# Kernel tuning notes

Measured on AMD Instinct MI355X. Metric: run time of the kernel, lower is better.

## Reference

```python
import jax, jax.numpy as jnp
import numpy as np

B, S, H = 4, 2048, 1024
NH, HD = 16, 64  # num heads, head dim


def setup_inputs() -> dict:
    key = jax.random.key(0)
    ks = jax.random.split(key, 8)
    s = 1.0 / np.sqrt(H)
    return {
        "hidden_states": jax.random.normal(ks[0], (B, S, H), jnp.float32),
        "attention_mask": jnp.zeros((B, 1, 1, S), jnp.float32),
        "Wq": jax.random.normal(ks[1], (H, H), jnp.float32) * s,
        "bq": jnp.zeros((H,), jnp.float32),
        "Wk": jax.random.normal(ks[2], (H, H), jnp.float32) * s,
        "bk": jnp.zeros((H,), jnp.float32),
        "Wv": jax.random.normal(ks[3], (H, H), jnp.float32) * s,
        "bv": jnp.zeros((H,), jnp.float32),
    }


def _split_heads(x):
    # [B, S, H] -> [B, NH, S, HD]
    return x.reshape(B, S, NH, HD).transpose(0, 2, 1, 3)


def reference(hidden_states, attention_mask, Wq, bq, Wk, bk, Wv, bv):
    q = _split_heads(hidden_states @ Wq + bq)
    k = _split_heads(hidden_states @ Wk + bk)
    v = _split_heads(hidden_states @ Wv + bv)
    scores = jnp.einsum("bhqd,bhkd->bhqk", q, k) / jnp.sqrt(jnp.float32(HD))
    probs = jax.nn.softmax(scores + attention_mask, axis=-1)  # dropout p=0 -> identity
    ctx = jnp.einsum("bhqk,bhkd->bhqd", probs, v)
    ctx = ctx.transpose(0, 2, 1, 3).reshape(B, S, H)
    return (ctx,)
```

## Files before the change

### kernel.cpp

```cpp
#include <hip/hip_runtime.h>
#include <hip/hip_bf16.h>
#include <stdint.h>


typedef unsigned short ushort_t;
typedef __attribute__((ext_vector_type(4))) float f32x4;
typedef __attribute__((ext_vector_type(8))) short short8;
typedef __attribute__((ext_vector_type(2))) unsigned int uint2v;

#define MFMA16(a, b, c) __builtin_amdgcn_mfma_f32_16x16x32_bf16((a), (b), (c), 0, 0, 0)

__device__ __forceinline__ ushort_t f2bf(float f) {
  unsigned u = __float_as_uint(f);
  u = (u + 0x7FFFu + ((u >> 16) & 1u)) >> 16;
  return (ushort_t)u;
}

typedef __attribute__((address_space(1))) unsigned int as1_uint;
typedef __attribute__((address_space(3))) unsigned int as3_uint;

__device__ __forceinline__ void async16(void* lds_dst, const void* g_src) {
  __builtin_amdgcn_global_load_lds((as1_uint*)(uintptr_t)g_src,
                                   (as3_uint*)(unsigned)(uintptr_t)lds_dst, 16, 0, 0);
}

__global__ __launch_bounds__(256) void convert_x(const float* __restrict__ X,
                                                 ushort_t* __restrict__ Xb) {
  int idx = (blockIdx.x * 256 + threadIdx.x) * 8;
  f32x4 a = *(const f32x4*)(X + idx);
  f32x4 b = *(const f32x4*)(X + idx + 4);
  short8 r;
#pragma unroll
  for (int j = 0; j < 4; ++j) r[j] = (short)f2bf(a[j]);
#pragma unroll
  for (int j = 0; j < 4; ++j) r[4 + j] = (short)f2bf(b[j]);
  *(short8*)(Xb + idx) = r;
}

__global__ __launch_bounds__(256) void convert_w(const float* __restrict__ Wq,
                                                 const float* __restrict__ Wk,
                                                 const float* __restrict__ Wv,
                                                 ushort_t* __restrict__ Wt) {
  const int mat = blockIdx.z;
  const float* W = (mat == 0) ? Wq : ((mat == 1) ? Wk : Wv);
  const int k0 = blockIdx.x * 64, n0 = blockIdx.y * 64;
  __shared__ float t[64][65];
  const int tid = threadIdx.x;
#pragma unroll
  for (int it = 0; it < 16; ++it) {
    int idx = it * 256 + tid;
    int r = idx >> 6, c = idx & 63;
    t[r][c] = W[(size_t)(k0 + r) * 1024 + n0 + c];
  }
  __syncthreads();
#pragma unroll
  for (int it = 0; it < 16; ++it) {
    int idx = it * 256 + tid;
    int nr = idx >> 6, kc = idx & 63;
    Wt[(size_t)(mat * 1024 + n0 + nr) * 1024 + k0 + kc] = f2bf(t[kc][nr]);
  }
}

__global__ __launch_bounds__(256) void gemm_qkv(const ushort_t* __restrict__ Xb,
                                                const ushort_t* __restrict__ Wt,
                                                const float* __restrict__ bq,
                                                const float* __restrict__ bk,
                                                const float* __restrict__ bv,
                                                ushort_t* __restrict__ Qb,
                                                ushort_t* __restrict__ Kb,
                                                ushort_t* __restrict__ Vt) {
  __shared__ char lds[36864];
  const int tid = threadIdx.x;
  const int l = tid & 63, w = tid >> 6;
  const int m0 = blockIdx.x * 128;
  const int n0 = blockIdx.y * 128;
  const int wm = w >> 1, wn = w & 1;

  const int lr = l >> 3;
  const int kb_log = (((l & 7) ^ lr) << 4);
  const char* srcA = (const char*)Xb + (size_t)(m0 + w * 32 + lr) * 2048 + kb_log;
  const char* srcB = (const char*)Wt + (size_t)(n0 + w * 32 + lr) * 2048 + kb_log;
  char* ldsA_w = lds + w * 4096;
  char* ldsB_w = lds + 16384 + w * 4096;

  const int ra = wm * 64 + (l & 15);
  const int rb = wn * 64 + (l & 15);
  const int swz = (l & 7) << 4;
  const int x0 = (((l >> 4) << 4)) ^ swz;
  const int x1 = (64 + ((l >> 4) << 4)) ^ swz;

  f32x4 acc[4][4];
#pragma unroll
  for (int mf = 0; mf < 4; ++mf)
#pragma unroll
    for (int nf = 0; nf < 4; ++nf) acc[mf][nf] = (f32x4){0.f, 0.f, 0.f, 0.f};

#pragma unroll 1
  for (int kt = 0; kt < 16; ++kt) {
    if (kt) __syncthreads();
    const int koff = kt * 128;
#pragma unroll
    for (int c = 0; c < 4; ++c) {
      async16(ldsA_w + c * 1024, srcA + c * 16384 + koff);
      async16(ldsB_w + c * 1024, srcB + c * 16384 + koff);
    }
    __syncthreads();
#pragma unroll
    for (int half = 0; half < 2; ++half) {
      const int xo = half ? x1 : x0;
      short8 av[4], bv2[4];
#pragma unroll
      for (int mf = 0; mf < 4; ++mf)
        av[mf] = *(const short8*)(lds + (ra + mf * 16) * 128 + xo);
#pragma unroll
      for (int nf = 0; nf < 4; ++nf)
        bv2[nf] = *(const short8*)(lds + 16384 + (rb + nf * 16) * 128 + xo);
#pragma unroll
      for (int mf = 0; mf < 4; ++mf)
#pragma unroll
        for (int nf = 0; nf < 4; ++nf)
          acc[mf][nf] = MFMA16(av[mf], bv2[nf], acc[mf][nf]);
    }
  }

  __syncthreads();
  const int col0 = n0 + wn * 64;
  const int mat = col0 >> 10;
  const int nn0 = col0 & 1023;
  const int hh = nn0 >> 6;
  const int row0 = m0 + wm * 64;
  const int bb = row0 >> 11;
  const int s0 = row0 & 2047;
  const float* bias = (mat == 0) ? bq : ((mat == 1) ? bk : bv);
  const float qscale = 0.18033688011112042f;
  if (mat < 2) {
    ushort_t* dst = (mat == 0) ? Qb : Kb;
    const float scl = (mat == 0) ? qscale : 1.0f;
#pragma unroll
    for (int mf = 0; mf < 4; ++mf)
#pragma unroll
      for (int nf = 0; nf < 4; ++nf)
#pragma unroll
        for (int i = 0; i < 4; ++i) {
          int r = mf * 16 + (l >> 4) * 4 + i;
          int d = nf * 16 + (l & 15);
          float v = (acc[mf][nf][i] + bias[nn0 + d]) * scl;
          dst[((size_t)(bb * 16 + hh) * 2048 + (s0 + r)) * 64 + d] = f2bf(v);
        }
  } else {
    ushort_t* vw = (ushort_t*)(lds + w * 9216);
#pragma unroll
    for (int mf = 0; mf < 4; ++mf)
#pragma unroll
      for (int nf = 0; nf < 4; ++nf)
#pragma unroll
        for (int i = 0; i < 4; ++i) {
          int r = mf * 16 + (l >> 4) * 4 + i;
          int d = nf * 16 + (l & 15);
          float v = acc[mf][nf][i] + bias[nn0 + d];
          vw[d * 72 + r] = f2bf(v);
        }
#pragma unroll
    for (int it = 0; it < 8; ++it) {
      int dr = it * 8 + (l >> 3);
      int sc = (l & 7) * 8;
      short8 vv = *(const short8*)((const char*)vw + dr * 144 + sc * 2);
      *(short8*)((char*)Vt + (((size_t)(bb * 16 + hh) * 64 + dr) * 2048 + s0 + sc) * 2) = vv;
    }
  }
}

__global__ __launch_bounds__(256) void attn_fwd(const ushort_t* __restrict__ Qb,
                                                const ushort_t* __restrict__ Kb,
                                                const ushort_t* __restrict__ Vt,
                                                const float* __restrict__ mask,
                                                float* __restrict__ out) {
  __shared__ char lds[49408];
  const int tid = threadIdx.x, l = tid & 63, w = tid >> 6;
  const int bh = blockIdx.y;
  const int bb = bh >> 4, hh = bh & 15;
  const int q0 = blockIdx.x * 64;
  const int lg = l >> 4, lr = l & 15;
  char* klds = lds;
  char* vlds = lds + 16384;
  char* pl = lds + 32768 + w * 2048;
  float* ml = (float*)(lds + 40960);
  float* sbuf = (float*)(lds + 49152 + w * 64);

  const float LOG2E = 1.44269504088896340736f;
  const f32x4 fzero = (f32x4){0.f, 0.f, 0.f, 0.f};
  const int psz = (lr & 7) << 4;

  const char* qbase = (const char*)Qb + ((size_t)bh * 2048 + q0 + w * 16 + lr) * 128 + lg * 16;
  short8 aq0 = *(const short8*)(qbase);
  short8 aq1 = *(const short8*)(qbase + 64);

  const int srow = l >> 3;
  const int scol = ((l & 7) ^ srow) << 4;
  const char* ksrc0 = (const char*)Kb + (size_t)bh * 2048 * 128 + (size_t)(w * 16 + srow) * 128 + scol;
  const char* vsrc0 = (const char*)Vt + ((size_t)bh * 64 + w * 16 + srow) * 4096 + scol;

  {
    char* kd = klds + w * 2048;
    char* vd = vlds + w * 2048;
    async16(kd, ksrc0);
    async16(kd + 1024, ksrc0 + 1024);
    async16(vd, vsrc0);
    async16(vd + 1024, vsrc0 + 8 * 4096);
  }
  {
    const float* mrow = mask + (size_t)bb * 2048;
    int mi = tid * 8;
    f32x4 a = *(const f32x4*)(mrow + mi);
    f32x4 b = *(const f32x4*)(mrow + mi + 4);
#pragma unroll
    for (int j = 0; j < 4; ++j) { a[j] *= LOG2E; b[j] *= LOG2E; }
    *(f32x4*)(ml + mi) = a;
    *(f32x4*)(ml + mi + 4) = b;
  }

  f32x4 lsum = fzero;
  f32x4 o[4];
#pragma unroll
  for (int vf = 0; vf < 4; ++vf) o[vf] = fzero;

#pragma unroll 1
  for (int kt = 0; kt < 32; ++kt) {
    const int cur = kt & 1;
    asm volatile("s_waitcnt lgkmcnt(0)" ::: "memory");
    __builtin_amdgcn_s_barrier();
    if (kt < 31) {
      char* kd = klds + (cur ^ 1) * 8192 + w * 2048;
      char* vd = vlds + (cur ^ 1) * 8192 + w * 2048;
      const char* ks = ksrc0 + (size_t)(kt + 1) * 8192;
      const char* vs = vsrc0 + (kt + 1) * 128;
      async16(kd, ks);
      async16(kd + 1024, ks + 1024);
      async16(vd, vs);
      async16(vd + 1024, vs + 8 * 4096);
      asm volatile("s_waitcnt vmcnt(4)" ::: "memory");
    } else {
      asm volatile("s_waitcnt vmcnt(0)" ::: "memory");
    }
    __builtin_amdgcn_s_barrier();
    __builtin_amdgcn_sched_barrier(0);

    const char* kb = klds + cur * 8192;
    const char* vb = vlds + cur * 8192;

#pragma unroll
    for (int kf = 0; kf < 4; ++kf) {
      const char* ka = kb + (kf * 16 + lr) * 128;
      short8 a0 = *(const short8*)(ka + ((lg * 16) ^ psz));
      short8 a1 = *(const short8*)(ka + ((64 + lg * 16) ^ psz));
      f32x4 s = MFMA16(a0, aq0, fzero);
      s = MFMA16(a1, aq1, s);
      f32x4 m4 = *(const f32x4*)(ml + kt * 64 + kf * 16 + lg * 4);
      f32x4 ps;
#pragma unroll
      for (int i = 0; i < 4; ++i) ps[i] = __builtin_amdgcn_exp2f(s[i] + m4[i]);
      lsum += ps;
      unsigned w0, w1;
      asm("v_cvt_pk_bf16_f32 %0, %1, %2" : "=v"(w0) : "v"(ps[0]), "v"(ps[1]));
      asm("v_cvt_pk_bf16_f32 %0, %1, %2" : "=v"(w1) : "v"(ps[2]), "v"(ps[3]));
      uint2v pw2 = {w0, w1};
      *(uint2v*)(pl + lr * 128 + ((kf * 32 + lg * 8) ^ psz)) = pw2;
    }

    short8 pa0 = *(const short8*)(pl + lr * 128 + ((lg * 16) ^ psz));
    short8 pa1 = *(const short8*)(pl + lr * 128 + ((64 + lg * 16) ^ psz));
#pragma unroll
    for (int vf = 0; vf < 4; ++vf) {
      const char* vrow = vb + (vf * 16 + lr) * 128;
      short8 v0 = *(const short8*)(vrow + ((lg * 16) ^ psz));
      short8 v1 = *(const short8*)(vrow + ((64 + lg * 16) ^ psz));
      o[vf] = MFMA16(pa0, v0, o[vf]);
      o[vf] = MFMA16(pa1, v1, o[vf]);
    }
  }

  float lrun = (lsum[0] + lsum[1]) + (lsum[2] + lsum[3]);
  lrun += __shfl_xor(lrun, 16);
  lrun += __shfl_xor(lrun, 32);
  if (lg == 0) sbuf[lr] = lrun;
  f32x4 l4 = *(const f32x4*)(sbuf + lg * 4);
  f32x4 inv4;
#pragma unroll
  for (int i = 0; i < 4; ++i) inv4[i] = 1.0f / l4[i];
#pragma unroll
  for (int vf = 0; vf < 4; ++vf)
#pragma unroll
    for (int i = 0; i < 4; ++i)
      out[((size_t)bb * 2048 + q0 + w * 16 + lg * 4 + i) * 1024 + hh * 64 + vf * 16 + lr] =
          o[vf][i] * inv4[i];
}

extern "C" void kernel_launch(void* const* d_in, const int* in_sizes, int n_in,
                              void* d_out, int out_size, void* d_ws, size_t ws_size,
                              hipStream_t stream) {
  const float* hs  = (const float*)d_in[0];
  const float* msk = (const float*)d_in[1];
  const float* Wq  = (const float*)d_in[2];
  const float* bq  = (const float*)d_in[3];
  const float* Wk  = (const float*)d_in[4];
  const float* bk  = (const float*)d_in[5];
  const float* Wv  = (const float*)d_in[6];
  const float* bv  = (const float*)d_in[7];
  float* out = (float*)d_out;
  char* ws = (char*)d_ws;
  ushort_t* Xb = (ushort_t*)ws;
  ushort_t* Wt = (ushort_t*)(ws + (16u << 20));
  ushort_t* Qb = (ushort_t*)(ws + (22u << 20));
  ushort_t* Kb = (ushort_t*)(ws + (38u << 20));
  ushort_t* Vt = (ushort_t*)(ws + (54u << 20));

  convert_x<<<4096, 256, 0, stream>>>(hs, Xb);
  convert_w<<<dim3(16, 16, 3), 256, 0, stream>>>(Wq, Wk, Wv, Wt);
  gemm_qkv<<<dim3(64, 24), 256, 0, stream>>>(Xb, Wt, bq, bk, bv, Qb, Kb, Vt);
  attn_fwd<<<dim3(32, 64), 256, 0, stream>>>(Qb, Kb, Vt, msk, out);
}
```

Before: 279.3 us.

## Process two query tiles per wave in attention to reuse K/V LDS loads

```diff
diff --git a/kernel.cpp b/kernel.cpp
--- a/kernel.cpp
+++ b/kernel.cpp
@@ -175,25 +175,27 @@
                                                 const ushort_t* __restrict__ Vt,
                                                 const float* __restrict__ mask,
                                                 float* __restrict__ out) {
-  __shared__ char lds[49408];
+  __shared__ char lds[49664];
   const int tid = threadIdx.x, l = tid & 63, w = tid >> 6;
   const int bh = blockIdx.y;
   const int bb = bh >> 4, hh = bh & 15;
-  const int q0 = blockIdx.x * 64;
+  const int q0 = blockIdx.x * 128;
   const int lg = l >> 4, lr = l & 15;
   char* klds = lds;
   char* vlds = lds + 16384;
-  char* pl = lds + 32768 + w * 2048;
-  float* ml = (float*)(lds + 40960);
-  float* sbuf = (float*)(lds + 49152 + w * 64);
+  char* pl = lds + 32768 + w * 4096;
+  float* sbuf = (float*)(lds + 49152 + w * 128);
 
   const float LOG2E = 1.44269504088896340736f;
   const f32x4 fzero = (f32x4){0.f, 0.f, 0.f, 0.f};
   const int psz = (lr & 7) << 4;
 
-  const char* qbase = (const char*)Qb + ((size_t)bh * 2048 + q0 + w * 16 + lr) * 128 + lg * 16;
-  short8 aq0 = *(const short8*)(qbase);
-  short8 aq1 = *(const short8*)(qbase + 64);
+  const char* qbase = (const char*)Qb + ((size_t)bh * 2048 + q0 + w * 32 + lr) * 128 + lg * 16;
+  short8 aq[2][2];
+  aq[0][0] = *(const short8*)(qbase);
+  aq[0][1] = *(const short8*)(qbase + 64);
+  aq[1][0] = *(const short8*)(qbase + 16 * 128);
+  aq[1][1] = *(const short8*)(qbase + 16 * 128 + 64);
 
   const int srow = l >> 3;
   const int scol = ((l & 7) ^ srow) << 4;
@@ -208,21 +210,17 @@
     async16(vd, vsrc0);
     async16(vd + 1024, vsrc0 + 8 * 4096);
   }
-  {
-    const float* mrow = mask + (size_t)bb * 2048;
-    int mi = tid * 8;
-    f32x4 a = *(const f32x4*)(mrow + mi);
-    f32x4 b = *(const f32x4*)(mrow + mi + 4);
-#pragma unroll
-    for (int j = 0; j < 4; ++j) { a[j] *= LOG2E; b[j] *= LOG2E; }
-    *(f32x4*)(ml + mi) = a;
-    *(f32x4*)(ml + mi + 4) = b;
-  }
-
-  f32x4 lsum = fzero;
-  f32x4 o[4];
-#pragma unroll
-  for (int vf = 0; vf < 4; ++vf) o[vf] = fzero;
+
+  const float* mrow = mask + (size_t)bb * 2048;
+
+  f32x4 lsum[2];
+  lsum[0] = fzero;
+  lsum[1] = fzero;
+  f32x4 o[2][4];
+#pragma unroll
+  for (int qc = 0; qc < 2; ++qc)
+#pragma unroll
+    for (int vf = 0; vf < 4; ++vf) o[qc][vf] = fzero;
 
 #pragma unroll 1
   for (int kt = 0; kt < 32; ++kt) {
@@ -253,46 +251,65 @@
       const char* ka = kb + (kf * 16 + lr) * 128;
       short8 a0 = *(const short8*)(ka + ((lg * 16) ^ psz));
       short8 a1 = *(const short8*)(ka + ((64 + lg * 16) ^ psz));
-      f32x4 s = MFMA16(a0, aq0, fzero);
-      s = MFMA16(a1, aq1, s);
-      f32x4 m4 = *(const f32x4*)(ml + kt * 64 + kf * 16 + lg * 4);
-      f32x4 ps;
-#pragma unroll
-      for (int i = 0; i < 4; ++i) ps[i] = __builtin_amdgcn_exp2f(s[i] + m4[i]);
-      lsum += ps;
-      unsigned w0, w1;
-      asm("v_cvt_pk_bf16_f32 %0, %1, %2" : "=v"(w0) : "v"(ps[0]), "v"(ps[1]));
-      asm("v_cvt_pk_bf16_f32 %0, %1, %2" : "=v"(w1) : "v"(ps[2]), "v"(ps[3]));
-      uint2v pw2 = {w0, w1};
-      *(uint2v*)(pl + lr * 128 + ((kf * 32 + lg * 8) ^ psz)) = pw2;
-    }
-
-    short8 pa0 = *(const short8*)(pl + lr * 128 + ((lg * 16) ^ psz));
-    short8 pa1 = *(const short8*)(pl + lr * 128 + ((64 + lg * 16) ^ psz));
+      f32x4 m4 = *(const f32x4*)(mrow + kt * 64 + kf * 16 + lg * 4);
+#pragma unroll
+      for (int qc = 0; qc < 2; ++qc) {
+        f32x4 s = MFMA16(a0, aq[qc][0], fzero);
+        s = MFMA16(a1, aq[qc][1], s);
+        f32x4 ps;
+#pragma unroll
+        for (int i = 0; i < 4; ++i)
+          ps[i] = __builtin_amdgcn_exp2f(fmaf(m4[i], LOG2E, s[i]));
+        lsum[qc] += ps;
+        unsigned w0, w1;
+        asm("v_cvt_pk_bf16_f32 %0, %1, %2" : "=v"(w0) : "v"(ps[0]), "v"(ps[1]));
+        asm("v_cvt_pk_bf16_f32 %0, %1, %2" : "=v"(w1) : "v"(ps[2]), "v"(ps[3]));
+        uint2v pw2 = {w0, w1};
+        *(uint2v*)(pl + (qc * 16 + lr) * 128 + ((kf * 32 + lg * 8) ^ psz)) = pw2;
+      }
+    }
+
+    short8 pa[2][2];
+#pragma unroll
+    for (int qc = 0; qc < 2; ++qc) {
+      pa[qc][0] = *(const short8*)(pl + (qc * 16 + lr) * 128 + ((lg * 16) ^ psz));
+      pa[qc][1] = *(const short8*)(pl + (qc * 16 + lr) * 128 + ((64 + lg * 16) ^ psz));
+    }
+    __builtin_amdgcn_s_setprio(1);
 #pragma unroll
     for (int vf = 0; vf < 4; ++vf) {
       const char* vrow = vb + (vf * 16 + lr) * 128;
       short8 v0 = *(const short8*)(vrow + ((lg * 16) ^ psz));
       short8 v1 = *(const short8*)(vrow + ((64 + lg * 16) ^ psz));
-      o[vf] = MFMA16(pa0, v0, o[vf]);
-      o[vf] = MFMA16(pa1, v1, o[vf]);
-    }
-  }
-
-  float lrun = (lsum[0] + lsum[1]) + (lsum[2] + lsum[3]);
-  lrun += __shfl_xor(lrun, 16);
-  lrun += __shfl_xor(lrun, 32);
-  if (lg == 0) sbuf[lr] = lrun;
-  f32x4 l4 = *(const f32x4*)(sbuf + lg * 4);
-  f32x4 inv4;
-#pragma unroll
-  for (int i = 0; i < 4; ++i) inv4[i] = 1.0f / l4[i];
-#pragma unroll
-  for (int vf = 0; vf < 4; ++vf)
-#pragma unroll
-    for (int i = 0; i < 4; ++i)
-      out[((size_t)bb * 2048 + q0 + w * 16 + lg * 4 + i) * 1024 + hh * 64 + vf * 16 + lr] =
-          o[vf][i] * inv4[i];
+#pragma unroll
+      for (int qc = 0; qc < 2; ++qc) {
+        o[qc][vf] = MFMA16(pa[qc][0], v0, o[qc][vf]);
+        o[qc][vf] = MFMA16(pa[qc][1], v1, o[qc][vf]);
+      }
+    }
+    __builtin_amdgcn_s_setprio(0);
+  }
+
+#pragma unroll
+  for (int qc = 0; qc < 2; ++qc) {
+    float lrun = (lsum[qc][0] + lsum[qc][1]) + (lsum[qc][2] + lsum[qc][3]);
+    lrun += __shfl_xor(lrun, 16);
+    lrun += __shfl_xor(lrun, 32);
+    if (lg == 0) sbuf[qc * 16 + lr] = lrun;
+  }
+#pragma unroll
+  for (int qc = 0; qc < 2; ++qc) {
+    f32x4 l4 = *(const f32x4*)(sbuf + qc * 16 + lg * 4);
+    f32x4 inv4;
+#pragma unroll
+    for (int i = 0; i < 4; ++i) inv4[i] = 1.0f / l4[i];
+#pragma unroll
+    for (int vf = 0; vf < 4; ++vf)
+#pragma unroll
+      for (int i = 0; i < 4; ++i)
+        out[((size_t)bb * 2048 + q0 + w * 32 + qc * 16 + lg * 4 + i) * 1024 + hh * 64 +
+            vf * 16 + lr] = o[qc][vf][i] * inv4[i];
+  }
 }
 
 extern "C" void kernel_launch(void* const* d_in, const int* in_sizes, int n_in,
@@ -317,5 +334,5 @@
   convert_x<<<4096, 256, 0, stream>>>(hs, Xb);
   convert_w<<<dim3(16, 16, 3), 256, 0, stream>>>(Wq, Wk, Wv, Wt);
   gemm_qkv<<<dim3(64, 24), 256, 0, stream>>>(Xb, Wt, bq, bk, bv, Qb, Kb, Vt);
-  attn_fwd<<<dim3(32, 64), 256, 0, stream>>>(Qb, Kb, Vt, msk, out);
-}
+  attn_fwd<<<dim3(16, 64), 256, 0, stream>>>(Qb, Kb, Vt, msk, out);
+}
```

After: 279.0 us. Within noise of the previous version (-0.1%).
